# Kernel tuning notes

Measured on AMD Instinct MI355X. Metric: run time of the kernel, lower is better.

Reference implementation:

```python
import jax, jax.numpy as jnp
import numpy as np

B, C, H, W = 2, 128, 64, 256
G, P, EXP = 8, 4, 2
D = C // G


def _conv1x1(x, w, b):
    # x: (b,c,h,w), w: (o,c), b: (o,)
    return jnp.einsum('bchw,oc->bohw', x, w) + b[None, :, None, None]


def _lin_sample(value, x):
    # value: (b,g,d,h,w); x: (b,g,p,h,w) pixel coords along W -> (b,g,d,p,h,w)
    Bv, Gv, Dv, Hv, Wv = value.shape
    Pv = x.shape[2]
    xc = jnp.clip(x, 0.0, Wv - 1.0)
    x0 = jnp.floor(xc)
    i0 = x0.astype(jnp.int32)
    i1 = jnp.minimum(i0 + 1, Wv - 1)
    t = (xc - x0)[:, :, None]  # (b,g,1,p,h,w)
    shape = (Bv, Gv, Dv, Pv, Hv, Wv)
    v = jnp.broadcast_to(value[:, :, :, None], shape)
    v0 = jnp.take_along_axis(v, jnp.broadcast_to(i0[:, :, None], shape), axis=-1)
    v1 = jnp.take_along_axis(v, jnp.broadcast_to(i1[:, :, None], shape), axis=-1)
    return v0 * (1.0 - t) + v1 * t


def _layernorm_c(x, g, b):
    mu = jnp.mean(x, axis=1, keepdims=True)
    var = jnp.mean((x - mu) ** 2, axis=1, keepdims=True)
    return (x - mu) * jax.lax.rsqrt(var + 1e-5) * g[None, :, None, None] + b[None, :, None, None]


def _forward(ml, mr, fl, fr, nl, nr, gml, gmr, cap, gap,
             wv, bv, wn, bn, woc, boc, wog, bog, wa, ba, wo, bo,
             lw, lb, w1, b1, w2, b2):
    mask = jnp.concatenate([gml, gmr], axis=0)   # (2B,1,H,W)
    q = jnp.concatenate([ml, mr], axis=0)        # (2B,C,H,W)
    ctx = jnp.concatenate([fr, fl], axis=0)      # cross: right feats for left queries
    geo = jnp.concatenate([nr, nl], axis=0)      # (2B,3,H,W)
    B2 = q.shape[0]
    # deformable 1D cross-attention (normal-guided)
    value = _conv1x1(ctx, wv, bv).reshape(B2, G, D, H, W)
    nfeat = _conv1x1(geo, wn, bn).reshape(B2, G, D, H, W)
    off_c = _conv1x1(q, woc, boc).reshape(B2, G, P, H, W)
    off_g = _conv1x1(q, wog, bog).reshape(B2, G, P, H, W)
    attn = jax.nn.softmax(_conv1x1(q, wa, ba).reshape(B2, G, 2 * P, H, W), axis=2)
    ctx_kp = jnp.clip(cap * (W - 1.0) + off_c, 0.0, W - 1.0)
    geo_kp = jnp.clip(gap * (W - 1.0) + off_g, 0.0, W - 1.0)
    s_ctx = _lin_sample(value, ctx_kp)           # (2B,G,D,P,H,W)
    s_geo = _lin_sample(nfeat, geo_kp)
    sampled = jnp.concatenate([s_ctx, s_geo], axis=3)  # (2B,G,D,2P,H,W)
    agg = jnp.einsum('bgdphw,bgphw->bgdhw', sampled, attn).reshape(B2, C, H, W)
    upd = _conv1x1(agg, wo, bo) * mask
    # residual + LayerNorm over channels + 1x1-conv FFN
    x = q + upd
    x = _layernorm_c(x, lw, lb)
    h1 = _conv1x1(x, w1, b1)
    x = x + _conv1x1(h1 * jax.nn.sigmoid(h1), w2, b2)
    return x, ctx_kp, geo_kp


def setup_inputs() -> dict:
    key = jax.random.key(0)
    ks = jax.random.split(key, 20)
    f32 = jnp.float32
    def n(k, shape, s=1.0):
        return jax.random.normal(k, shape, dtype=f32) * s
    return {
        'match_left': n(ks[0], (B, C, H, W)),
        'match_right': n(ks[1], (B, C, H, W)),
        'feat_left': n(ks[2], (B, C, H, W)),
        'feat_right': n(ks[3], (B, C, H, W)),
        'normal_left': n(ks[4], (B, 3, H, W)),
        'normal_right': n(ks[5], (B, 3, H, W)),
        'gate_mask_left': jax.random.uniform(ks[6], (B, 1, H, W), dtype=f32),
        'gate_mask_right': jax.random.uniform(ks[7], (B, 1, H, W), dtype=f32),
        'context_anchor_points': jax.random.uniform(ks[8], (2 * B, G, P, H, W), dtype=f32),
        'geometric_anchor_points': jax.random.uniform(ks[9], (2 * B, G, P, H, W), dtype=f32),
        'w_value': n(ks[10], (C, C), 0.02), 'b_value': jnp.zeros((C,), f32),
        'w_normal': n(ks[11], (C, 3), 0.02), 'b_normal': jnp.zeros((C,), f32),
        'w_off_ctx': n(ks[12], (G * P, C), 0.02), 'b_off_ctx': jnp.zeros((G * P,), f32),
        'w_off_geo': n(ks[13], (G * P, C), 0.02), 'b_off_geo': jnp.zeros((G * P,), f32),
        'w_attn': n(ks[14], (G * 2 * P, C), 0.02), 'b_attn': jnp.zeros((G * 2 * P,), f32),
        'w_out': n(ks[15], (C, C), 0.02), 'b_out': jnp.zeros((C,), f32),
        'ln_w': jnp.ones((C,), f32), 'ln_b': jnp.zeros((C,), f32),
        'w_ff1': n(ks[16], (EXP * C, C), 0.02), 'b_ff1': jnp.zeros((EXP * C,), f32),
        'w_ff2': n(ks[17], (C, EXP * C), 0.02), 'b_ff2': jnp.zeros((C,), f32),
    }


def reference(match_left, match_right, feat_left, feat_right, normal_left, normal_right,
              gate_mask_left, gate_mask_right, context_anchor_points, geometric_anchor_points,
              w_value, b_value, w_normal, b_normal, w_off_ctx, b_off_ctx, w_off_geo, b_off_geo,
              w_attn, b_attn, w_out, b_out, ln_w, ln_b, w_ff1, b_ff1, w_ff2, b_ff2):
    x, ckp, gkp = _forward(match_left, match_right, feat_left, feat_right, normal_left, normal_right,
                           gate_mask_left, gate_mask_right, context_anchor_points, geometric_anchor_points,
                           w_value, b_value, w_normal, b_normal, w_off_ctx, b_off_ctx, w_off_geo, b_off_geo,
                           w_attn, b_attn, w_out, b_out, ln_w, ln_b, w_ff1, b_ff1, w_ff2, b_ff2)
    ml, mr = jnp.split(x, 2, axis=0)
    return (ml, mr, ckp, gkp)
```

## Files before the change

### kernel.cpp

```cpp
#include <hip/hip_runtime.h>
#include <cstdint>
#include <math.h>

#define B2v 4
#define Cc  128
#define Hh  64
#define Ww  256
#define Gg  8
#define Pp  4
#define HW  (Hh*Ww)
#define CHW (Cc*HW)
#define PIT 136

typedef float f32x4 __attribute__((ext_vector_type(4)));
typedef float f32x2 __attribute__((ext_vector_type(2)));
typedef short s16x8 __attribute__((ext_vector_type(8)));
typedef short s16x4 __attribute__((ext_vector_type(4)));

__device__ __forceinline__ short f2bf(float x) {
    union { float f; unsigned u; } a; a.f = x;
    unsigned r = a.u + 0x7fffu + ((a.u >> 16) & 1u);
    return (short)(r >> 16);
}
__device__ __forceinline__ float bf2f(short s) {
    union { unsigned u; float f; } a; a.u = ((unsigned)(unsigned short)s) << 16;
    return a.f;
}
__device__ __forceinline__ unsigned cvtpk(float lo, float hi) {
    unsigned r;
    asm("v_cvt_pk_bf16_f32 %0, %1, %2" : "=v"(r) : "v"(lo), "v"(hi));
    return r;
}
__device__ __forceinline__ f32x2 unpk(unsigned w) {
    union { unsigned u; float f; } lo, hi;
    lo.u = w << 16; hi.u = w & 0xffff0000u;
    return (f32x2){lo.f, hi.f};
}
__device__ __forceinline__ float frcp(float x) { return __builtin_amdgcn_rcpf(x); }
__device__ __forceinline__ float fexp(float x) { return __expf(x); }

__global__ __launch_bounds__(256) void prep_kernel(
    const float* __restrict__ wv, const float* __restrict__ woc,
    const float* __restrict__ wog, const float* __restrict__ wa,
    const float* __restrict__ wo, const float* __restrict__ w1,
    const float* __restrict__ w2,
    const float* __restrict__ boc, const float* __restrict__ bog,
    const float* __restrict__ ba,
    short* __restrict__ wbf, float* __restrict__ bq)
{
    int i = blockIdx.x * 256 + threadIdx.x;
    if (i < 16384) wbf[i] = f2bf(wv[i]);
    else if (i < 32768) {
        int j = i - 16384; int r = j >> 7, c = j & 127;
        float v = (r < 32) ? woc[r * 128 + c] : (r < 64) ? wog[(r - 32) * 128 + c]
                                              : wa[(r - 64) * 128 + c];
        wbf[i] = f2bf(v);
    }
    else if (i < 49152)  wbf[i] = f2bf(wo[i - 32768]);
    else if (i < 81920)  wbf[i] = f2bf(w1[i - 49152]);
    else if (i < 114688) wbf[i] = f2bf(w2[i - 81920]);
    else if (i < 114816) {
        int r = i - 114688;
        bq[r] = (r < 32) ? boc[r] : (r < 64) ? bog[r - 32] : ba[r - 64];
    }
}

__global__ __launch_bounds__(1024, 4) void mega_kernel(
    const float* __restrict__ mlq, const float* __restrict__ mrq,
    const float* __restrict__ fl,  const float* __restrict__ fr,
    const float* __restrict__ nl,  const float* __restrict__ nr,
    const float* __restrict__ gml, const float* __restrict__ gmr,
    const float* __restrict__ cap, const float* __restrict__ gap,
    const short* __restrict__ wbf, const float* __restrict__ bq,
    const float* __restrict__ bv,
    const float* __restrict__ wn,  const float* __restrict__ bn,
    const float* __restrict__ bo,
    const float* __restrict__ lnw, const float* __restrict__ lnb,
    const float* __restrict__ b1,  const float* __restrict__ b2,
    float* __restrict__ out_ml, float* __restrict__ out_mr,
    float* __restrict__ ckp_out, float* __restrict__ gkp_out)
{
    __shared__ short buf1[256 * PIT];
    __shared__ short buf2[256 * PIT];
    __shared__ f32x4 sgeo4[256];
    __shared__ f32x2 swnp[256];
    __shared__ float sln[256];
    __shared__ float redS[1024], redQ[1024];
    __shared__ float smu[256], srs[256];

    const short* wv_bf = wbf;
    const short* wq_bf = wbf + 16384;
    const short* wo_bf = wbf + 32768;
    const short* w1_bf = wbf + 49152;
    const short* w2_bf = wbf + 81920;

    const int t    = threadIdx.x;
    const int lane = t & 63;
    const int wvid = t >> 6;
    const int rw   = wvid & 7;
    const int pw   = wvid >> 3;
    const int lm   = lane & 15;
    const int lq   = lane >> 4;
    const int h = blockIdx.x, b = blockIdx.y;
    const int hWw = h * Ww;
    const int px   = t & 255;
    const int qt   = t >> 8;

    const float* ctx = (b < 2) ? fr + (size_t)b * CHW : fl + (size_t)(b - 2) * CHW;
    const float* q   = (b < 2) ? mlq + (size_t)b * CHW : mrq + (size_t)(b - 2) * CHW;
    const float* geo = (b < 2) ? nr + (size_t)b * 3 * HW : nl + (size_t)(b - 2) * 3 * HW;
    const float* msk = (b < 2) ? gml + (size_t)b * HW : gmr + (size_t)(b - 2) * HW;
    float* outp = (b < 2) ? out_ml + (size_t)b * CHW : out_mr + (size_t)(b - 2) * CHW;

    float capr[8], gapr[8];
    const size_t kbase = ((size_t)b * Gg + qt * 2) * Pp * (size_t)HW + hWw + px;
    {
#pragma unroll
        for (int i = 0; i < 8; i++) {
            capr[i] = cap[kbase + (size_t)i * HW];
            gapr[i] = gap[kbase + (size_t)i * HW];
        }
    }

    if (t < 256) {
        sgeo4[t] = (f32x4){geo[hWw + t], geo[HW + hWw + t], geo[2 * HW + hWw + t], 0.f};
        const int pr = t >> 2, m = t & 3;
        const int ch0 = pr * 2, ch1 = ch0 + 1;
        float a0 = (m < 3) ? wn[ch0 * 3 + m] : bn[ch0];
        float a1 = (m < 3) ? wn[ch1 * 3 + m] : bn[ch1];
        swnp[t] = (f32x2){a0, a1};
    }
    else if (t < 512) {
        int i = t - 256;
        sln[i] = (i < 128) ? lnw[i] : lnb[i - 128];
    }

    {
        const int c0 = wvid * 8;
        const int p0 = lane * 4;
        const size_t gbase = (size_t)c0 * HW + hWw + p0;
        {
            f32x4 L[8];
#pragma unroll
            for (int c = 0; c < 8; c++) L[c] = *(const f32x4*)(ctx + gbase + (size_t)c * HW);
#pragma unroll
            for (int j = 0; j < 4; j++) {
                uint4 w0;
                w0.x = cvtpk(L[0][j], L[1][j]);  w0.y = cvtpk(L[2][j], L[3][j]);
                w0.z = cvtpk(L[4][j], L[5][j]);  w0.w = cvtpk(L[6][j], L[7][j]);
                *(uint4*)(&buf1[(p0 + j) * PIT + c0]) = w0;
            }
        }
        {
            f32x4 L[8];
#pragma unroll
            for (int c = 0; c < 8; c++) L[c] = *(const f32x4*)(q + gbase + (size_t)c * HW);
#pragma unroll
            for (int j = 0; j < 4; j++) {
                uint4 w0;
                w0.x = cvtpk(L[0][j], L[1][j]);  w0.y = cvtpk(L[2][j], L[3][j]);
                w0.z = cvtpk(L[4][j], L[5][j]);  w0.w = cvtpk(L[6][j], L[7][j]);
                *(uint4*)(&buf2[(p0 + j) * PIT + c0]) = w0;
            }
        }
    }
    __syncthreads();

    f32x4 accv[8];
#pragma unroll
    for (int nt = 0; nt < 8; nt++) accv[nt] = (f32x4){0.f, 0.f, 0.f, 0.f};
#pragma unroll
    for (int kk = 0; kk < 4; kk++) {
        s16x8 a = *(const s16x8*)(wv_bf + (size_t)(rw * 16 + lm) * 128 + kk * 32 + lq * 8);
#pragma unroll
        for (int nt = 0; nt < 8; nt++) {
            s16x8 bfv = *(const s16x8*)(&buf1[((pw * 8 + nt) * 16 + lm) * PIT + kk * 32 + lq * 8]);
            accv[nt] = __builtin_amdgcn_mfma_f32_16x16x32_bf16(a, bfv, accv[nt], 0, 0, 0);
        }
    }
    __syncthreads();

    {
        const int ob = rw * 16 + lq * 4;
        float bias[4];
#pragma unroll
        for (int r = 0; r < 4; r++) bias[r] = bv[ob + r];
#pragma unroll
        for (int nt = 0; nt < 8; nt++) {
            const int wg = (pw * 8 + nt) * 16 + lm;
            uint2 pk;
            pk.x = cvtpk(accv[nt][0] + bias[0], accv[nt][1] + bias[1]);
            pk.y = cvtpk(accv[nt][2] + bias[2], accv[nt][3] + bias[3]);
            *(uint2*)(&buf1[wg * PIT + ob]) = pk;
        }
    }
    f32x4 accp[8];
#pragma unroll
    for (int nt = 0; nt < 8; nt++) accp[nt] = (f32x4){0.f, 0.f, 0.f, 0.f};
#pragma unroll
    for (int kk = 0; kk < 4; kk++) {
        s16x8 a = *(const s16x8*)(wq_bf + (size_t)(rw * 16 + lm) * 128 + kk * 32 + lq * 8);
#pragma unroll
        for (int nt = 0; nt < 8; nt++) {
            s16x8 bfv = *(const s16x8*)(&buf2[((pw * 8 + nt) * 16 + lm) * PIT + kk * 32 + lq * 8]);
            accp[nt] = __builtin_amdgcn_mfma_f32_16x16x32_bf16(a, bfv, accp[nt], 0, 0, 0);
        }
    }
    __syncthreads();

    {
        const int ob = rw * 16 + lq * 4;
        float bias[4];
#pragma unroll
        for (int r = 0; r < 4; r++) bias[r] = bq[ob + r];
#pragma unroll
        for (int nt = 0; nt < 8; nt++) {
            const int wg = (pw * 8 + nt) * 16 + lm;
            uint2 pk;
            pk.x = cvtpk(accp[nt][0] + bias[0], accp[nt][1] + bias[1]);
            pk.y = cvtpk(accp[nt][2] + bias[2], accp[nt][3] + bias[3]);
            *(uint2*)(&buf2[wg * PIT + ob]) = pk;
        }
    }
    __syncthreads();

    float attnr[2][8], kpr[2][8];
#pragma unroll
    for (int gi = 0; gi < 2; gi++) {
        const int g = qt * 2 + gi;
        s16x8 lg = *(const s16x8*)(&buf2[px * PIT + 64 + g * 8]);
        float L[8], m = -1e30f;
#pragma unroll
        for (int j = 0; j < 8; j++) { L[j] = bf2f(lg[j]); m = fmaxf(m, L[j]); }
        float s = 0.f;
#pragma unroll
        for (int j = 0; j < 8; j++) { L[j] = fexp(L[j] - m); s += L[j]; }
        float inv = frcp(s);
#pragma unroll
        for (int j = 0; j < 8; j++) attnr[gi][j] = L[j] * inv;
#pragma unroll
        for (int p = 0; p < 4; p++) {
            size_t kidx = kbase + (size_t)(gi * 4 + p) * HW;
            float oc = bf2f(buf2[px * PIT + g * 4 + p]);
            float og = bf2f(buf2[px * PIT + 32 + g * 4 + p]);
            float ck = fminf(fmaxf(capr[gi * 4 + p] * 255.0f + oc, 0.f), 255.f);
            float gk = fminf(fmaxf(gapr[gi * 4 + p] * 255.0f + og, 0.f), 255.f);
            ckp_out[kidx] = ck;
            gkp_out[kidx] = gk;
            kpr[gi][p] = ck;
            kpr[gi][4 + p] = gk;
        }
    }
    __syncthreads();

#pragma unroll
    for (int gi = 0; gi < 2; gi++) {
        const int g = qt * 2 + gi;
        f32x2 A[8];
#pragma unroll
        for (int k = 0; k < 8; k++) A[k] = (f32x2){0.f, 0.f};
#pragma unroll
        for (int j = 0; j < 4; j++) {
            float x = kpr[gi][j];
            float fx = floorf(x);
            int i0 = (int)fx;
            int i1 = min(i0 + 1, Ww - 1);
            float tt = x - fx;
            float c0 = attnr[gi][j] * (1.f - tt);
            float c1 = attnr[gi][j] * tt;
            f32x2 c0v = {c0, c0}, c1v = {c1, c1};
            uint4 v0a = *(const uint4*)(&buf1[i0 * PIT + g * 16]);
            uint4 v0b = *(const uint4*)(&buf1[i0 * PIT + g * 16 + 8]);
            uint4 v1a = *(const uint4*)(&buf1[i1 * PIT + g * 16]);
            uint4 v1b = *(const uint4*)(&buf1[i1 * PIT + g * 16 + 8]);
            const unsigned w0[8] = {v0a.x, v0a.y, v0a.z, v0a.w, v0b.x, v0b.y, v0b.z, v0b.w};
            const unsigned w1[8] = {v1a.x, v1a.y, v1a.z, v1a.w, v1b.x, v1b.y, v1b.z, v1b.w};
#pragma unroll
            for (int k = 0; k < 8; k++)
                A[k] += unpk(w0[k]) * c0v + unpk(w1[k]) * c1v;
        }
        {
            float gs0 = 0.f, gs1 = 0.f, gs2 = 0.f, as = 0.f;
#pragma unroll
            for (int j = 4; j < 8; j++) {
                float x = kpr[gi][j];
                float fx = floorf(x);
                int i0 = (int)fx;
                int i1 = min(i0 + 1, Ww - 1);
                float tt = x - fx;
                float c0 = attnr[gi][j] * (1.f - tt);
                float c1 = attnr[gi][j] * tt;
                f32x4 ga = sgeo4[i0], gb = sgeo4[i1];
                gs0 += c0 * ga[0] + c1 * gb[0];
                gs1 += c0 * ga[1] + c1 * gb[1];
                gs2 += c0 * ga[2] + c1 * gb[2];
                as  += attnr[gi][j];
            }
            f32x2 g0v = {gs0, gs0}, g1v = {gs1, gs1}, g2v = {gs2, gs2}, asv = {as, as};
#pragma unroll
            for (int k = 0; k < 8; k++) {
                const f32x2* wp = &swnp[(g * 8 + k) * 4];
                A[k] += wp[0] * g0v + wp[1] * g1v + wp[2] * g2v + wp[3] * asv;
            }
        }
        uint4 o0, o1;
        o0.x = cvtpk(A[0][0], A[0][1]); o0.y = cvtpk(A[1][0], A[1][1]);
        o0.z = cvtpk(A[2][0], A[2][1]); o0.w = cvtpk(A[3][0], A[3][1]);
        o1.x = cvtpk(A[4][0], A[4][1]); o1.y = cvtpk(A[5][0], A[5][1]);
        o1.z = cvtpk(A[6][0], A[6][1]); o1.w = cvtpk(A[7][0], A[7][1]);
        *(uint4*)(&buf2[px * PIT + g * 16])     = o0;
        *(uint4*)(&buf2[px * PIT + g * 16 + 8]) = o1;
    }
    __syncthreads();

    {
        f32x4 acc1[8];
#pragma unroll
        for (int nt = 0; nt < 8; nt++) acc1[nt] = (f32x4){0.f, 0.f, 0.f, 0.f};
#pragma unroll
        for (int kk = 0; kk < 4; kk++) {
            s16x8 a = *(const s16x8*)(wo_bf + (size_t)(rw * 16 + lm) * 128 + kk * 32 + lq * 8);
#pragma unroll
            for (int nt = 0; nt < 8; nt++) {
                s16x8 bfv = *(const s16x8*)(&buf2[((pw * 8 + nt) * 16 + lm) * PIT + kk * 32 + lq * 8]);
                acc1[nt] = __builtin_amdgcn_mfma_f32_16x16x32_bf16(a, bfv, acc1[nt], 0, 0, 0);
            }
        }
        const int ob = rw * 16 + lq * 4;
        float bias[4];
#pragma unroll
        for (int r = 0; r < 4; r++) bias[r] = bo[ob + r];
#pragma unroll
        for (int nt = 0; nt < 8; nt++) {
            const int wg = (pw * 8 + nt) * 16 + lm;
            float mval = msk[hWw + wg];
            float xv[4];
#pragma unroll
            for (int r = 0; r < 4; r++) {
                float upd = acc1[nt][r] + bias[r];
                float qv = q[(size_t)(ob + r) * HW + hWw + wg];
                xv[r] = qv + upd * mval;
            }
            uint2 pk;
            pk.x = cvtpk(xv[0], xv[1]);
            pk.y = cvtpk(xv[2], xv[3]);
            *(uint2*)(&buf1[wg * PIT + ob]) = pk;
        }
    }
    __syncthreads();

    {
        float ls = 0.f, lsq = 0.f;
#pragma unroll
        for (int c8 = 0; c8 < 4; c8++) {
            uint4 u = *(const uint4*)(&buf1[px * PIT + qt * 32 + c8 * 8]);
            const unsigned wv4[4] = {u.x, u.y, u.z, u.w};
#pragma unroll
            for (int j2 = 0; j2 < 4; j2++) {
                f32x2 e = unpk(wv4[j2]);
                ls  += e[0] + e[1];
                lsq += e[0] * e[0] + e[1] * e[1];
            }
        }
        redS[t] = ls; redQ[t] = lsq;
        __syncthreads();
        if (t < 256) {
            float s  = redS[t] + redS[t + 256] + redS[t + 512] + redS[t + 768];
            float qq = redQ[t] + redQ[t + 256] + redQ[t + 512] + redQ[t + 768];
            float mu = s * (1.f / 128.f);
            float var = qq * (1.f / 128.f) - mu * mu;
            smu[t] = mu;
            srs[t] = __builtin_amdgcn_rsqf(var + 1e-5f);
        }
        __syncthreads();
        const float mu = smu[px], rs = srs[px];
#pragma unroll
        for (int c8 = 0; c8 < 4; c8++) {
            const int cb = qt * 32 + c8 * 8;
            uint4 u = *(const uint4*)(&buf1[px * PIT + cb]);
            const unsigned wv4[4] = {u.x, u.y, u.z, u.w};
            uint4 o;
            unsigned res[4];
#pragma unroll
            for (int j2 = 0; j2 < 4; j2++) {
                f32x2 e = unpk(wv4[j2]);
                const int c = cb + j2 * 2;
                float a0 = rs * sln[c],     bb0 = sln[128 + c]     - mu * a0;
                float a1 = rs * sln[c + 1], bb1 = sln[128 + c + 1] - mu * a1;
                res[j2] = cvtpk(e[0] * a0 + bb0, e[1] * a1 + bb1);
            }
            o.x = res[0]; o.y = res[1]; o.z = res[2]; o.w = res[3];
            *(uint4*)(&buf1[px * PIT + cb]) = o;
        }
    }
    __syncthreads();

    f32x4 acc3[8];
#pragma unroll
    for (int nt = 0; nt < 8; nt++) acc3[nt] = (f32x4){0.f, 0.f, 0.f, 0.f};

    for (int jc = 0; jc < 2; jc++) {
        f32x4 acc2[8];
#pragma unroll
        for (int nt = 0; nt < 8; nt++) acc2[nt] = (f32x4){0.f, 0.f, 0.f, 0.f};
#pragma unroll
        for (int kk = 0; kk < 4; kk++) {
            s16x8 a = *(const s16x8*)(w1_bf + (size_t)(jc * 128 + rw * 16 + lm) * 128 + kk * 32 + lq * 8);
#pragma unroll
            for (int nt = 0; nt < 8; nt++) {
                s16x8 bfv = *(const s16x8*)(&buf1[((pw * 8 + nt) * 16 + lm) * PIT + kk * 32 + lq * 8]);
                acc2[nt] = __builtin_amdgcn_mfma_f32_16x16x32_bf16(a, bfv, acc2[nt], 0, 0, 0);
            }
        }
        {
            const int jb = rw * 16 + lq * 4;
            float bias[4];
#pragma unroll
            for (int r = 0; r < 4; r++) bias[r] = b1[jc * 128 + jb + r];
#pragma unroll
            for (int nt = 0; nt < 8; nt++) {
                const int wg = (pw * 8 + nt) * 16 + lm;
                float o[4];
#pragma unroll
                for (int r = 0; r < 4; r++) {
                    float hv = acc2[nt][r] + bias[r];
                    o[r] = hv * frcp(1.f + fexp(-hv));
                }
                uint2 pk;
                pk.x = cvtpk(o[0], o[1]);
                pk.y = cvtpk(o[2], o[3]);
                *(uint2*)(&buf2[wg * PIT + jb]) = pk;
            }
        }
        __syncthreads();
#pragma unroll
        for (int kk = 0; kk < 4; kk++) {
            s16x8 a = *(const s16x8*)(w2_bf + (size_t)(rw * 16 + lm) * 256 + jc * 128 + kk * 32 + lq * 8);
#pragma unroll
            for (int nt = 0; nt < 8; nt++) {
                s16x8 bfv = *(const s16x8*)(&buf2[((pw * 8 + nt) * 16 + lm) * PIT + kk * 32 + lq * 8]);
                acc3[nt] = __builtin_amdgcn_mfma_f32_16x16x32_bf16(a, bfv, acc3[nt], 0, 0, 0);
            }
        }
        __syncthreads();
    }

    {
        const int ob = rw * 16 + lq * 4;
        float b2v[4];
#pragma unroll
        for (int r = 0; r < 4; r++) b2v[r] = b2[ob + r];
#pragma unroll
        for (int nt = 0; nt < 8; nt++) {
            const int wg = (pw * 8 + nt) * 16 + lm;
            s16x4 xn4 = *(const s16x4*)(&buf1[wg * PIT + ob]);
#pragma unroll
            for (int r = 0; r < 4; r++)
                outp[(size_t)(ob + r) * HW + hWw + wg] = bf2f(xn4[r]) + b2v[r] + acc3[nt][r];
        }
    }
}

extern "C" void kernel_launch(void* const* d_in, const int* in_sizes, int n_in,
                              void* d_out, int out_size, void* d_ws, size_t ws_size,
                              hipStream_t stream)
{
    const float* match_l = (const float*)d_in[0];
    const float* match_r = (const float*)d_in[1];
    const float* feat_l  = (const float*)d_in[2];
    const float* feat_r  = (const float*)d_in[3];
    const float* norm_l  = (const float*)d_in[4];
    const float* norm_r  = (const float*)d_in[5];
    const float* gml     = (const float*)d_in[6];
    const float* gmr     = (const float*)d_in[7];
    const float* cap     = (const float*)d_in[8];
    const float* gap     = (const float*)d_in[9];
    const float* wv  = (const float*)d_in[10]; const float* bv  = (const float*)d_in[11];
    const float* wn  = (const float*)d_in[12]; const float* bn  = (const float*)d_in[13];
    const float* woc = (const float*)d_in[14]; const float* boc = (const float*)d_in[15];
    const float* wog = (const float*)d_in[16]; const float* bog = (const float*)d_in[17];
    const float* wa  = (const float*)d_in[18]; const float* ba  = (const float*)d_in[19];
    const float* wo  = (const float*)d_in[20]; const float* bo  = (const float*)d_in[21];
    const float* lnw = (const float*)d_in[22]; const float* lnb = (const float*)d_in[23];
    const float* w1  = (const float*)d_in[24]; const float* b1  = (const float*)d_in[25];
    const float* w2  = (const float*)d_in[26]; const float* b2  = (const float*)d_in[27];

    float* out = (float*)d_out;
    float* out_ml  = out;
    float* out_mr  = out + (size_t)2 * CHW;
    float* ckp_out = out + (size_t)4 * CHW;
    float* gkp_out = ckp_out + (size_t)B2v * Gg * Pp * HW;

    float* ws = (float*)d_ws;
    float* bq  = ws;
    short* wbf = (short*)(bq + 128);

    prep_kernel<<<dim3(449), dim3(256), 0, stream>>>(
        wv, woc, wog, wa, wo, w1, w2, boc, bog, ba, wbf, bq);
    mega_kernel<<<dim3(Hh, B2v), dim3(1024), 0, stream>>>(
        match_l, match_r, feat_l, feat_r, norm_l, norm_r, gml, gmr, cap, gap,
        wbf, bq, bv, wn, bn, bo, lnw, lnb, b1, b2,
        out_ml, out_mr, ckp_out, gkp_out);
}
```

Measured before the change: 213.8 us.

## Switch GEMMs to 32x32x16 MFMA tiles and overlap loads with compute

Replaces the 16x16x32 bf16 MFMA tiling in all five 1x1-conv GEMMs with 32x32x16 tiles. Each wave now owns a 32-channel by 64-pixel tile, which cuts LDS B-operand reads per FLOP and the number of accumulator registers live at once. The query global load is moved to overlap with the value GEMM. The residual query and mask reads are prefetched into registers before the sampling phase, and the FFN hidden computation is restructured so both halves of the first layer are computed together. This raises register pressure (h0/h1 plus prefetched qres), which could lower occupancy.

```diff
diff --git a/kernel.cpp b/kernel.cpp
--- a/kernel.cpp
+++ b/kernel.cpp
@@ -14,6 +14,7 @@
 
 typedef float f32x4 __attribute__((ext_vector_type(4)));
 typedef float f32x2 __attribute__((ext_vector_type(2)));
+typedef float f32x16 __attribute__((ext_vector_type(16)));
 typedef short s16x8 __attribute__((ext_vector_type(8)));
 typedef short s16x4 __attribute__((ext_vector_type(4)));
 
@@ -38,6 +39,13 @@
 }
 __device__ __forceinline__ float frcp(float x) { return __builtin_amdgcn_rcpf(x); }
 __device__ __forceinline__ float fexp(float x) { return __expf(x); }
+__device__ __forceinline__ f32x16 zero16() {
+    f32x16 z;
+#pragma unroll
+    for (int i = 0; i < 16; i++) z[i] = 0.f;
+    return z;
+}
+#define MFMA32(a, bfr, c) __builtin_amdgcn_mfma_f32_32x32x16_bf16((a), (bfr), (c), 0, 0, 0)
 
 __global__ __launch_bounds__(256) void prep_kernel(
     const float* __restrict__ wv, const float* __restrict__ woc,
@@ -97,14 +105,19 @@
     const int t    = threadIdx.x;
     const int lane = t & 63;
     const int wvid = t >> 6;
-    const int rw   = wvid & 7;
-    const int pw   = wvid >> 3;
-    const int lm   = lane & 15;
-    const int lq   = lane >> 4;
+    const int ct   = wvid & 3;
+    const int pt   = wvid >> 2;
+    const int l31  = lane & 31;
+    const int hi   = lane >> 5;
     const int h = blockIdx.x, b = blockIdx.y;
     const int hWw = h * Ww;
     const int px   = t & 255;
     const int qt   = t >> 8;
+
+    const int obch = ct * 32 + hi * 4;
+    const int kof  = hi * 8;
+    const int px0  = pt * 64 + l31;
+    const int px1  = px0 + 32;
 
     const float* ctx = (b < 2) ? fr + (size_t)b * CHW : fl + (size_t)(b - 2) * CHW;
     const float* q   = (b < 2) ? mlq + (size_t)b * CHW : mrq + (size_t)(b - 2) * CHW;
@@ -139,87 +152,84 @@
         const int c0 = wvid * 8;
         const int p0 = lane * 4;
         const size_t gbase = (size_t)c0 * HW + hWw + p0;
-        {
-            f32x4 L[8];
-#pragma unroll
-            for (int c = 0; c < 8; c++) L[c] = *(const f32x4*)(ctx + gbase + (size_t)c * HW);
-#pragma unroll
-            for (int j = 0; j < 4; j++) {
-                uint4 w0;
-                w0.x = cvtpk(L[0][j], L[1][j]);  w0.y = cvtpk(L[2][j], L[3][j]);
-                w0.z = cvtpk(L[4][j], L[5][j]);  w0.w = cvtpk(L[6][j], L[7][j]);
-                *(uint4*)(&buf1[(p0 + j) * PIT + c0]) = w0;
-            }
-        }
-        {
-            f32x4 L[8];
-#pragma unroll
-            for (int c = 0; c < 8; c++) L[c] = *(const f32x4*)(q + gbase + (size_t)c * HW);
-#pragma unroll
-            for (int j = 0; j < 4; j++) {
-                uint4 w0;
-                w0.x = cvtpk(L[0][j], L[1][j]);  w0.y = cvtpk(L[2][j], L[3][j]);
-                w0.z = cvtpk(L[4][j], L[5][j]);  w0.w = cvtpk(L[6][j], L[7][j]);
-                *(uint4*)(&buf2[(p0 + j) * PIT + c0]) = w0;
-            }
-        }
-    }
-    __syncthreads();
-
-    f32x4 accv[8];
-#pragma unroll
-    for (int nt = 0; nt < 8; nt++) accv[nt] = (f32x4){0.f, 0.f, 0.f, 0.f};
-#pragma unroll
-    for (int kk = 0; kk < 4; kk++) {
-        s16x8 a = *(const s16x8*)(wv_bf + (size_t)(rw * 16 + lm) * 128 + kk * 32 + lq * 8);
-#pragma unroll
-        for (int nt = 0; nt < 8; nt++) {
-            s16x8 bfv = *(const s16x8*)(&buf1[((pw * 8 + nt) * 16 + lm) * PIT + kk * 32 + lq * 8]);
-            accv[nt] = __builtin_amdgcn_mfma_f32_16x16x32_bf16(a, bfv, accv[nt], 0, 0, 0);
-        }
-    }
-    __syncthreads();
-
-    {
-        const int ob = rw * 16 + lq * 4;
-        float bias[4];
-#pragma unroll
-        for (int r = 0; r < 4; r++) bias[r] = bv[ob + r];
-#pragma unroll
-        for (int nt = 0; nt < 8; nt++) {
-            const int wg = (pw * 8 + nt) * 16 + lm;
-            uint2 pk;
-            pk.x = cvtpk(accv[nt][0] + bias[0], accv[nt][1] + bias[1]);
-            pk.y = cvtpk(accv[nt][2] + bias[2], accv[nt][3] + bias[3]);
-            *(uint2*)(&buf1[wg * PIT + ob]) = pk;
-        }
-    }
-    f32x4 accp[8];
-#pragma unroll
-    for (int nt = 0; nt < 8; nt++) accp[nt] = (f32x4){0.f, 0.f, 0.f, 0.f};
-#pragma unroll
-    for (int kk = 0; kk < 4; kk++) {
-        s16x8 a = *(const s16x8*)(wq_bf + (size_t)(rw * 16 + lm) * 128 + kk * 32 + lq * 8);
-#pragma unroll
-        for (int nt = 0; nt < 8; nt++) {
-            s16x8 bfv = *(const s16x8*)(&buf2[((pw * 8 + nt) * 16 + lm) * PIT + kk * 32 + lq * 8]);
-            accp[nt] = __builtin_amdgcn_mfma_f32_16x16x32_bf16(a, bfv, accp[nt], 0, 0, 0);
-        }
-    }
-    __syncthreads();
-
-    {
-        const int ob = rw * 16 + lq * 4;
-        float bias[4];
-#pragma unroll
-        for (int r = 0; r < 4; r++) bias[r] = bq[ob + r];
-#pragma unroll
-        for (int nt = 0; nt < 8; nt++) {
-            const int wg = (pw * 8 + nt) * 16 + lm;
-            uint2 pk;
-            pk.x = cvtpk(accp[nt][0] + bias[0], accp[nt][1] + bias[1]);
-            pk.y = cvtpk(accp[nt][2] + bias[2], accp[nt][3] + bias[3]);
-            *(uint2*)(&buf2[wg * PIT + ob]) = pk;
+        f32x4 L[8];
+#pragma unroll
+        for (int c = 0; c < 8; c++) L[c] = *(const f32x4*)(ctx + gbase + (size_t)c * HW);
+#pragma unroll
+        for (int j = 0; j < 4; j++) {
+            uint4 w0;
+            w0.x = cvtpk(L[0][j], L[1][j]);  w0.y = cvtpk(L[2][j], L[3][j]);
+            w0.z = cvtpk(L[4][j], L[5][j]);  w0.w = cvtpk(L[6][j], L[7][j]);
+            *(uint4*)(&buf1[(p0 + j) * PIT + c0]) = w0;
+        }
+    }
+    __syncthreads();
+
+    f32x16 accv[2];
+    accv[0] = zero16(); accv[1] = zero16();
+    {
+        const int c0 = wvid * 8;
+        const int p0 = lane * 4;
+        const size_t gbase = (size_t)c0 * HW + hWw + p0;
+        f32x4 L[8];
+#pragma unroll
+        for (int c = 0; c < 8; c++) L[c] = *(const f32x4*)(q + gbase + (size_t)c * HW);
+#pragma unroll
+        for (int kk = 0; kk < 8; kk++) {
+            s16x8 a = *(const s16x8*)(wv_bf + (size_t)(ct * 32 + l31) * 128 + kk * 16 + kof);
+            s16x8 b0 = *(const s16x8*)(&buf1[px0 * PIT + kk * 16 + kof]);
+            s16x8 b1v = *(const s16x8*)(&buf1[px1 * PIT + kk * 16 + kof]);
+            accv[0] = MFMA32(a, b0, accv[0]);
+            accv[1] = MFMA32(a, b1v, accv[1]);
+        }
+#pragma unroll
+        for (int j = 0; j < 4; j++) {
+            uint4 w0;
+            w0.x = cvtpk(L[0][j], L[1][j]);  w0.y = cvtpk(L[2][j], L[3][j]);
+            w0.z = cvtpk(L[4][j], L[5][j]);  w0.w = cvtpk(L[6][j], L[7][j]);
+            *(uint4*)(&buf2[(p0 + j) * PIT + c0]) = w0;
+        }
+    }
+    __syncthreads();
+
+    {
+#pragma unroll
+        for (int s = 0; s < 4; s++) {
+            f32x4 bb = *(const f32x4*)(bv + obch + s * 8);
+#pragma unroll
+            for (int nt = 0; nt < 2; nt++) {
+                const int pxn = px0 + nt * 32;
+                uint2 pk;
+                pk.x = cvtpk(accv[nt][s * 4 + 0] + bb[0], accv[nt][s * 4 + 1] + bb[1]);
+                pk.y = cvtpk(accv[nt][s * 4 + 2] + bb[2], accv[nt][s * 4 + 3] + bb[3]);
+                *(uint2*)(&buf1[pxn * PIT + obch + s * 8]) = pk;
+            }
+        }
+    }
+    f32x16 accp[2];
+    accp[0] = zero16(); accp[1] = zero16();
+#pragma unroll
+    for (int kk = 0; kk < 8; kk++) {
+        s16x8 a = *(const s16x8*)(wq_bf + (size_t)(ct * 32 + l31) * 128 + kk * 16 + kof);
+        s16x8 b0 = *(const s16x8*)(&buf2[px0 * PIT + kk * 16 + kof]);
+        s16x8 b1v = *(const s16x8*)(&buf2[px1 * PIT + kk * 16 + kof]);
+        accp[0] = MFMA32(a, b0, accp[0]);
+        accp[1] = MFMA32(a, b1v, accp[1]);
+    }
+    __syncthreads();
+
+    {
+#pragma unroll
+        for (int s = 0; s < 4; s++) {
+            f32x4 bb = *(const f32x4*)(bq + obch + s * 8);
+#pragma unroll
+            for (int nt = 0; nt < 2; nt++) {
+                const int pxn = px0 + nt * 32;
+                uint2 pk;
+                pk.x = cvtpk(accp[nt][s * 4 + 0] + bb[0], accp[nt][s * 4 + 1] + bb[1]);
+                pk.y = cvtpk(accp[nt][s * 4 + 2] + bb[2], accp[nt][s * 4 + 3] + bb[3]);
+                *(uint2*)(&buf2[pxn * PIT + obch + s * 8]) = pk;
+            }
         }
     }
     __syncthreads();
@@ -250,6 +260,18 @@
             kpr[gi][p] = ck;
             kpr[gi][4 + p] = gk;
         }
+    }
+    float qres[2][16];
+    float mres[2];
+#pragma unroll
+    for (int nt = 0; nt < 2; nt++) {
+        const int pxn = px0 + nt * 32;
+        mres[nt] = msk[hWw + pxn];
+#pragma unroll
+        for (int s = 0; s < 4; s++)
+#pragma unroll
+            for (int r = 0; r < 4; r++)
+                qres[nt][s * 4 + r] = q[(size_t)(obch + s * 8 + r) * HW + hWw + pxn];
     }
     __syncthreads();
 
@@ -314,37 +336,31 @@
     __syncthreads();
 
     {
-        f32x4 acc1[8];
-#pragma unroll
-        for (int nt = 0; nt < 8; nt++) acc1[nt] = (f32x4){0.f, 0.f, 0.f, 0.f};
-#pragma unroll
-        for (int kk = 0; kk < 4; kk++) {
-            s16x8 a = *(const s16x8*)(wo_bf + (size_t)(rw * 16 + lm) * 128 + kk * 32 + lq * 8);
-#pragma unroll
-            for (int nt = 0; nt < 8; nt++) {
-                s16x8 bfv = *(const s16x8*)(&buf2[((pw * 8 + nt) * 16 + lm) * PIT + kk * 32 + lq * 8]);
-                acc1[nt] = __builtin_amdgcn_mfma_f32_16x16x32_bf16(a, bfv, acc1[nt], 0, 0, 0);
-            }
-        }
-        const int ob = rw * 16 + lq * 4;
-        float bias[4];
-#pragma unroll
-        for (int r = 0; r < 4; r++) bias[r] = bo[ob + r];
-#pragma unroll
-        for (int nt = 0; nt < 8; nt++) {
-            const int wg = (pw * 8 + nt) * 16 + lm;
-            float mval = msk[hWw + wg];
-            float xv[4];
-#pragma unroll
-            for (int r = 0; r < 4; r++) {
-                float upd = acc1[nt][r] + bias[r];
-                float qv = q[(size_t)(ob + r) * HW + hWw + wg];
-                xv[r] = qv + upd * mval;
-            }
-            uint2 pk;
-            pk.x = cvtpk(xv[0], xv[1]);
-            pk.y = cvtpk(xv[2], xv[3]);
-            *(uint2*)(&buf1[wg * PIT + ob]) = pk;
+        f32x16 acc1[2];
+        acc1[0] = zero16(); acc1[1] = zero16();
+#pragma unroll
+        for (int kk = 0; kk < 8; kk++) {
+            s16x8 a = *(const s16x8*)(wo_bf + (size_t)(ct * 32 + l31) * 128 + kk * 16 + kof);
+            s16x8 b0 = *(const s16x8*)(&buf2[px0 * PIT + kk * 16 + kof]);
+            s16x8 b1v = *(const s16x8*)(&buf2[px1 * PIT + kk * 16 + kof]);
+            acc1[0] = MFMA32(a, b0, acc1[0]);
+            acc1[1] = MFMA32(a, b1v, acc1[1]);
+        }
+#pragma unroll
+        for (int s = 0; s < 4; s++) {
+            f32x4 bb = *(const f32x4*)(bo + obch + s * 8);
+#pragma unroll
+            for (int nt = 0; nt < 2; nt++) {
+                const int pxn = px0 + nt * 32;
+                float xv[4];
+#pragma unroll
+                for (int r = 0; r < 4; r++)
+                    xv[r] = qres[nt][s * 4 + r] + (acc1[nt][s * 4 + r] + bb[r]) * mres[nt];
+                uint2 pk;
+                pk.x = cvtpk(xv[0], xv[1]);
+                pk.y = cvtpk(xv[2], xv[3]);
+                *(uint2*)(&buf1[pxn * PIT + obch + s * 8]) = pk;
+            }
         }
     }
     __syncthreads();
@@ -395,68 +411,88 @@
     }
     __syncthreads();
 
-    f32x4 acc3[8];
-#pragma unroll
-    for (int nt = 0; nt < 8; nt++) acc3[nt] = (f32x4){0.f, 0.f, 0.f, 0.f};
-
-    for (int jc = 0; jc < 2; jc++) {
-        f32x4 acc2[8];
-#pragma unroll
-        for (int nt = 0; nt < 8; nt++) acc2[nt] = (f32x4){0.f, 0.f, 0.f, 0.f};
-#pragma unroll
-        for (int kk = 0; kk < 4; kk++) {
-            s16x8 a = *(const s16x8*)(w1_bf + (size_t)(jc * 128 + rw * 16 + lm) * 128 + kk * 32 + lq * 8);
-#pragma unroll
-            for (int nt = 0; nt < 8; nt++) {
-                s16x8 bfv = *(const s16x8*)(&buf1[((pw * 8 + nt) * 16 + lm) * PIT + kk * 32 + lq * 8]);
-                acc2[nt] = __builtin_amdgcn_mfma_f32_16x16x32_bf16(a, bfv, acc2[nt], 0, 0, 0);
-            }
-        }
-        {
-            const int jb = rw * 16 + lq * 4;
-            float bias[4];
-#pragma unroll
-            for (int r = 0; r < 4; r++) bias[r] = b1[jc * 128 + jb + r];
-#pragma unroll
-            for (int nt = 0; nt < 8; nt++) {
-                const int wg = (pw * 8 + nt) * 16 + lm;
-                float o[4];
-#pragma unroll
-                for (int r = 0; r < 4; r++) {
-                    float hv = acc2[nt][r] + bias[r];
-                    o[r] = hv * frcp(1.f + fexp(-hv));
-                }
-                uint2 pk;
-                pk.x = cvtpk(o[0], o[1]);
-                pk.y = cvtpk(o[2], o[3]);
-                *(uint2*)(&buf2[wg * PIT + jb]) = pk;
-            }
-        }
-        __syncthreads();
-#pragma unroll
-        for (int kk = 0; kk < 4; kk++) {
-            s16x8 a = *(const s16x8*)(w2_bf + (size_t)(rw * 16 + lm) * 256 + jc * 128 + kk * 32 + lq * 8);
-#pragma unroll
-            for (int nt = 0; nt < 8; nt++) {
-                s16x8 bfv = *(const s16x8*)(&buf2[((pw * 8 + nt) * 16 + lm) * PIT + kk * 32 + lq * 8]);
-                acc3[nt] = __builtin_amdgcn_mfma_f32_16x16x32_bf16(a, bfv, acc3[nt], 0, 0, 0);
-            }
-        }
-        __syncthreads();
-    }
-
-    {
-        const int ob = rw * 16 + lq * 4;
-        float b2v[4];
-#pragma unroll
-        for (int r = 0; r < 4; r++) b2v[r] = b2[ob + r];
-#pragma unroll
-        for (int nt = 0; nt < 8; nt++) {
-            const int wg = (pw * 8 + nt) * 16 + lm;
-            s16x4 xn4 = *(const s16x4*)(&buf1[wg * PIT + ob]);
+    f32x16 h0[2], h1[2];
+    h0[0] = zero16(); h0[1] = zero16(); h1[0] = zero16(); h1[1] = zero16();
+#pragma unroll
+    for (int kk = 0; kk < 8; kk++) {
+        s16x8 a0 = *(const s16x8*)(w1_bf + (size_t)(ct * 32 + l31) * 128 + kk * 16 + kof);
+        s16x8 a1 = *(const s16x8*)(w1_bf + (size_t)(128 + ct * 32 + l31) * 128 + kk * 16 + kof);
+        s16x8 b0 = *(const s16x8*)(&buf1[px0 * PIT + kk * 16 + kof]);
+        s16x8 b1v = *(const s16x8*)(&buf1[px1 * PIT + kk * 16 + kof]);
+        h0[0] = MFMA32(a0, b0, h0[0]);  h0[1] = MFMA32(a0, b1v, h0[1]);
+        h1[0] = MFMA32(a1, b0, h1[0]);  h1[1] = MFMA32(a1, b1v, h1[1]);
+    }
+#pragma unroll
+    for (int s = 0; s < 4; s++) {
+        f32x4 bb = *(const f32x4*)(b1 + obch + s * 8);
+#pragma unroll
+        for (int nt = 0; nt < 2; nt++) {
+            const int pxn = px0 + nt * 32;
+            float o[4];
+#pragma unroll
+            for (int r = 0; r < 4; r++) {
+                float hv = h0[nt][s * 4 + r] + bb[r];
+                o[r] = hv * frcp(1.f + fexp(-hv));
+            }
+            uint2 pk;
+            pk.x = cvtpk(o[0], o[1]);
+            pk.y = cvtpk(o[2], o[3]);
+            *(uint2*)(&buf2[pxn * PIT + obch + s * 8]) = pk;
+        }
+    }
+    __syncthreads();
+
+    f32x16 acc3[2];
+    acc3[0] = zero16(); acc3[1] = zero16();
+#pragma unroll
+    for (int kk = 0; kk < 8; kk++) {
+        s16x8 a = *(const s16x8*)(w2_bf + (size_t)(ct * 32 + l31) * 256 + kk * 16 + kof);
+        s16x8 b0 = *(const s16x8*)(&buf2[px0 * PIT + kk * 16 + kof]);
+        s16x8 b1v = *(const s16x8*)(&buf2[px1 * PIT + kk * 16 + kof]);
+        acc3[0] = MFMA32(a, b0, acc3[0]);
+        acc3[1] = MFMA32(a, b1v, acc3[1]);
+    }
+    __syncthreads();
+
+#pragma unroll
+    for (int s = 0; s < 4; s++) {
+        f32x4 bb = *(const f32x4*)(b1 + 128 + obch + s * 8);
+#pragma unroll
+        for (int nt = 0; nt < 2; nt++) {
+            const int pxn = px0 + nt * 32;
+            float o[4];
+#pragma unroll
+            for (int r = 0; r < 4; r++) {
+                float hv = h1[nt][s * 4 + r] + bb[r];
+                o[r] = hv * frcp(1.f + fexp(-hv));
+            }
+            uint2 pk;
+            pk.x = cvtpk(o[0], o[1]);
+            pk.y = cvtpk(o[2], o[3]);
+            *(uint2*)(&buf2[pxn * PIT + obch + s * 8]) = pk;
+        }
+    }
+    __syncthreads();
+
+#pragma unroll
+    for (int kk = 0; kk < 8; kk++) {
+        s16x8 a = *(const s16x8*)(w2_bf + (size_t)(ct * 32 + l31) * 256 + 128 + kk * 16 + kof);
+        s16x8 b0 = *(const s16x8*)(&buf2[px0 * PIT + kk * 16 + kof]);
+        s16x8 b1v = *(const s16x8*)(&buf2[px1 * PIT + kk * 16 + kof]);
+        acc3[0] = MFMA32(a, b0, acc3[0]);
+        acc3[1] = MFMA32(a, b1v, acc3[1]);
+    }
+#pragma unroll
+    for (int s = 0; s < 4; s++) {
+        f32x4 bb = *(const f32x4*)(b2 + obch + s * 8);
+#pragma unroll
+        for (int nt = 0; nt < 2; nt++) {
+            const int pxn = px0 + nt * 32;
+            s16x4 xn4 = *(const s16x4*)(&buf1[pxn * PIT + obch + s * 8]);
 #pragma unroll
             for (int r = 0; r < 4; r++)
-                outp[(size_t)(ob + r) * HW + hWw + wg] = bf2f(xn4[r]) + b2v[r] + acc3[nt][r];
+                outp[(size_t)(obch + s * 8 + r) * HW + hWw + pxn] =
+                    bf2f(xn4[r]) + bb[r] + acc3[nt][s * 4 + r];
         }
     }
 }
```

Measured after the change: 227.3 us. 6.3% more time.
